# Kernel tuning notes

Measured on AMD Instinct MI355X. Metric: run time of the kernel, lower is better.

The kernel has to match this reference:

```python
import jax, jax.numpy as jnp
import numpy as np

B, F, ND, H, H1, M, NSEL = 8192, 40, 10, 64, 16, 75, 60
GRU_L = 3


def setup_inputs() -> dict:
    key = jax.random.key(0)
    ks = iter(jax.random.split(key, 64))
    def nrm(shape, scale=1.0):
        return jax.random.normal(next(ks), shape, jnp.float32) * scale
    d = {}
    d["X"] = nrm((B, 22, F))
    d["A"] = jax.random.uniform(next(ks), (B, 22, 22), dtype=jnp.float32)
    FO = F + (F - ND)  # 70: tiled R features + node-specific features
    for br, fin in (("R", F), ("O", FO), ("D", FO)):
        d[f"Wg_{br}"] = nrm((fin, H), fin ** -0.5)
        d[f"bg_{br}"] = jnp.zeros((H,), jnp.float32)
    for br, gin in (("R", 2 * H), ("O", 3 * H), ("D", 2 * H)):
        d[f"Wz_{br}"] = nrm((gin, H), gin ** -0.5)
        d[f"Wr_{br}"] = nrm((gin, H), gin ** -0.5)
        d[f"Wm_{br}"] = nrm((gin, H), gin ** -0.5)
        d[f"bm_{br}"] = jnp.zeros((H,), jnp.float32)
    for br in "ROD":
        d[f"W1_{br}"] = nrm((H, H1), H ** -0.5)
        d[f"b1_{br}"] = jnp.zeros((H1,), jnp.float32)
        d[f"W2_{br}"] = nrm((H1, 1), H1 ** -0.5)
    # temporal branch: 3 role-specific learned season vectors + fwd/bwd 1-unit GRUs
    d["temporal"] = nrm((3, M), 0.1)
    d["gru_k"] = nrm((3, 2, 3))      # [branch, fwd/bwd, (z,r,h)] input kernels (input dim 1)
    d["gru_rk"] = nrm((3, 2, 3))     # recurrent kernels (units=1)
    d["gru_b"] = jnp.zeros((3, 2, 2, 3), jnp.float32)  # reset_after=True: input & recurrent bias
    d["wout"] = nrm((3,))            # output Dense(1, no bias) on 1-dim GRU output
    d["ys_succ_ind"] = jnp.sort(jax.random.randint(next(ks), (NSEL,), 0, M))
    return d


def _temporal_probs(t, k, rk, b, wo, idx):
    # t:[M]  k,rk:[2,3]  b:[2,2,3]  wo: scalar. Keras GRU (units=1, reset_after=True).
    def make_step(kk, rkk, bb):
        def step(h, x):
            z = jax.nn.sigmoid(x * kk[0] + bb[0, 0] + h * rkk[0] + bb[1, 0])
            r = jax.nn.sigmoid(x * kk[1] + bb[0, 1] + h * rkk[1] + bb[1, 1])
            hh = jnp.tanh(x * kk[2] + bb[0, 2] + r * (h * rkk[2] + bb[1, 2]))
            hn = z * h + (1.0 - z) * hh
            return hn, hn
        return step
    h0 = jnp.zeros((), t.dtype)
    _, f = jax.lax.scan(make_step(k[0], rk[0], b[0]), h0, t)          # forward GRU
    _, g = jax.lax.scan(make_step(k[1], rk[1], b[1]), h0, f[::-1])     # go_backwards GRU (keeps reversed order, as Keras)
    p = jax.nn.softmax(g * wo)   # softmax over M time steps
    return p[idx]                # gather successful-season indices -> [NSEL]


def _fwd(X, A, Wg_R, bg_R, Wg_O, bg_O, Wg_D, bg_D,
         Wz_R, Wr_R, Wm_R, bm_R, Wz_O, Wr_O, Wm_O, bm_O,
         Wz_D, Wr_D, Wm_D, bm_D,
         W1_R, b1_R, W2_R, W1_O, b1_O, W2_O, W1_D, b1_D, W2_D,
         temporal, gru_k, gru_rk, gru_b, wout, ys_succ_ind):
    X_R = X[:, :1, :]                                               # [B,1,F]
    X_O = jnp.concatenate([jnp.tile(X_R, (1, 10, 1)), X[:, 1:11, ND:]], -1)  # [B,10,FO]
    X_D = jnp.concatenate([jnp.tile(X_R, (1, 11, 1)), X[:, 11:, ND:]], -1)   # [B,11,FO]
    A_RO = A[:, :1, 1:11]    # R <- O  [B,1,10]
    A_OR = A[:, 1:11, :1]    # O <- R  [B,10,1]
    A_OD = A[:, 1:11, 11:]   # O <- D  [B,10,11]
    A_DO = A[:, 11:, 1:11]   # D <- O  [B,11,10]
    h_R = jnp.tanh(X_R @ Wg_R + bg_R)
    h_O = jnp.tanh(X_O @ Wg_O + bg_O)
    h_D = jnp.tanh(X_D @ Wg_D + bg_D)
    def gate(h, n, Wz, Wr, Wm, bm):
        hn = jnp.concatenate([h, n], -1)
        z = jax.nn.sigmoid(hn @ Wz)
        r = jax.nn.sigmoid(hn @ Wr)
        hm = jnp.tanh(jnp.concatenate([h * r, n], -1) @ Wm + bm)
        return (1.0 - z) * h + z * hm
    for _ in range(GRU_L):
        n_R = A_RO @ h_O                                            # [B,1,H]
        n_O = jnp.concatenate([A_OR @ h_R, A_OD @ h_D], -1)         # [B,10,2H]
        n_D = A_DO @ h_O                                            # [B,11,H]
        h_R = gate(h_R, n_R, Wz_R, Wr_R, Wm_R, bm_R)
        h_O = gate(h_O, n_O, Wz_O, Wr_O, Wm_O, bm_O)
        h_D = gate(h_D, n_D, Wz_D, Wr_D, Wm_D, bm_D)
    s_R = (jnp.tanh(h_R @ W1_R + b1_R) @ W2_R)[:, 0]                # squeeze node dim -> [B,1]
    s_O = jnp.sum(jnp.tanh(h_O @ W1_O + b1_O) @ W2_O, axis=1)       # [B,1]
    s_D = jnp.sum(jnp.tanh(h_D @ W1_D + b1_D) @ W2_D, axis=1)       # [B,1]
    tp = jax.vmap(_temporal_probs, in_axes=(0, 0, 0, 0, 0, None))(
        temporal, gru_k, gru_rk, gru_b, wout, ys_succ_ind)          # [3,NSEL]
    return s_R * tp[0] + s_O * tp[1] + s_D * tp[2]                  # [B,NSEL]


def reference(X, A, Wg_R, bg_R, Wg_O, bg_O, Wg_D, bg_D,
              Wz_R, Wr_R, Wm_R, bm_R, Wz_O, Wr_O, Wm_O, bm_O,
              Wz_D, Wr_D, Wm_D, bm_D,
              W1_R, b1_R, W2_R, W1_O, b1_O, W2_O, W1_D, b1_D, W2_D,
              temporal, gru_k, gru_rk, gru_b, wout, ys_succ_ind):
    return _fwd(X, A, Wg_R, bg_R, Wg_O, bg_O, Wg_D, bg_D,
                Wz_R, Wr_R, Wm_R, bm_R, Wz_O, Wr_O, Wm_O, bm_O,
                Wz_D, Wr_D, Wm_D, bm_D,
                W1_R, b1_R, W2_R, W1_O, b1_O, W2_O, W1_D, b1_D, W2_D,
                temporal, gru_k, gru_rk, gru_b, wout, ys_succ_ind)
```

## Files before the change

### kernel.cpp

```cpp
#include <hip/hip_runtime.h>
#include <hip/hip_bf16.h>
#include <math.h>

#define DEV __device__ __forceinline__

DEV float sigmoidf_(float x) { return 1.0f / (1.0f + __expf(-x)); }

#define L5A(OP) OP(0,0) OP(1,1) OP(2,2) OP(3,3) OP(4,4)
#define L5B(OP) OP(0,5) OP(1,6) OP(2,7) OP(3,8) OP(4,9)
#define L6A(OP) OP(0,0) OP(1,1) OP(2,2) OP(3,3) OP(4,4) OP(5,5)
#define L5D(OP) OP(0,6) OP(1,7) OP(2,8) OP(3,9) OP(4,10)

#define AROB 0
#define AORB 16
#define AODB 32
#define ADOB 144
#define ANUM 256

DEV float gstep(float x, float h, const float* k, const float* rk, const float* bb) {
  const float z  = sigmoidf_(fmaf(x, k[0], bb[0]) + fmaf(h, rk[0], bb[3]));
  const float r  = sigmoidf_(fmaf(x, k[1], bb[1]) + fmaf(h, rk[1], bb[4]));
  const float hh = tanhf(fmaf(x, k[2], bb[2]) + r * fmaf(h, rk[2], bb[5]));
  return z * h + (1.f - z) * hh;
}

__global__ void __launch_bounds__(64, 1)
// ... 41 lines not shown
  else if (fi < 144) { W = WzO; base = 96;  }
  else if (fi < 192) { W = WrO; base = 144; }
  else if (fi < 240) { W = WmO; base = 192; }
  else if (fi < 272) { W = WzD; base = 240; }
  else if (fi < 304) { W = WrD; base = 272; }
  else               { W = WmD; base = 304; }
  const int kb = fi - base;
  float4 v;
  v.x = W[(kb * 4 + 0) * 64 + c];
  v.y = W[(kb * 4 + 1) * 64 + c];
  v.z = W[(kb * 4 + 2) * 64 + c];
  v.w = W[(kb * 4 + 3) * 64 + c];
  *(float4*)(ws + 1024 + (size_t)fi * 1024 + c * 16) = v;
}

#define ZRDECL(s,i) float az##s = 0.f, ar##s = 0.f;
#define AORD(s,i)  const float aor##s = sA2[AORB + (i)];
#define OS0(s,i) { const float4 v = *reinterpret_cast<const float4*>(&hS[(1+(i))*64 + kb*4]); \
  az##s=fmaf(v.x,wz.x,az##s); az##s=fmaf(v.y,wz.y,az##s); az##s=fmaf(v.z,wz.z,az##s); az##s=fmaf(v.w,wz.w,az##s); \
  ar##s=fmaf(v.x,wr.x,ar##s); ar##s=fmaf(v.y,wr.y,ar##s); ar##s=fmaf(v.z,wr.z,ar##s); ar##s=fmaf(v.w,wr.w,ar##s); }
#define OS1(s,i) { az##s=fmaf(aor##s,uz.x,az##s); az##s=fmaf(aor##s,uz.y,az##s); \
  az##s=fmaf(aor##s,uz.z,az##s); az##s=fmaf(aor##s,uz.w,az##s); \
  ar##s=fmaf(aor##s,ur.x,ar##s); ar##s=fmaf(aor##s,ur.y,ar##s); \
  ar##s=fmaf(aor##s,ur.z,ar##s); ar##s=fmaf(aor##s,ur.w,ar##s); }
#define OS2(s,i) { const float4 v = *reinterpret_cast<const float4*>(&nS[(1+(i))*64 + (kb-32)*4]); \
  az##s=fmaf(v.x,wz.x,az##s); az##s=fmaf(v.y,wz.y,az##s); az##s=fmaf(v.z,wz.z,az##s); az##s=fmaf(v.w,wz.w,az##s); \
  ar##s=fmaf(v.x,wr.x,ar##s); ar##s=fmaf(v.y,wr.y,ar##s); ar##s=fmaf(v.z,wr.z,ar##s); ar##s=fmaf(v.w,wr.w,ar##s); }
#define OSIG(s,i) zS##s = sigmoidf_(az##s); const float rr##s = sigmoidf_(ar##s);
#define OGST(s,i) gS[(1+(i))*64+c] = hS[(1+(i))*64+c] * rr##s;
#define OAMD(s,i) aS##s = bmOc;
#define OM0(s,i) { const float4 v = *reinterpret_cast<const float4*>(&gS[(1+(i))*64 + kb*4]); \
  aS##s=fmaf(v.x,wm.x,aS##s); aS##s=fmaf(v.y,wm.y,aS##s); aS##s=fmaf(v.z,wm.z,aS##s); aS##s=fmaf(v.w,wm.w,aS##s); }
#define OM1(s,i) { aS##s=fmaf(aor##s,um.x,aS##s); aS##s=fmaf(aor##s,um.y,aS##s); \
  aS##s=fmaf(aor##s,um.z,aS##s); aS##s=fmaf(aor##s,um.w,aS##s); }
#define OM2(s,i) { const float4 v = *reinterpret_cast<const float4*>(&nS[(1+(i))*64 + (kb-32)*4]); \
  aS##s=fmaf(v.x,wm.x,aS##s); aS##s=fmaf(v.y,wm.y,aS##s); aS##s=fmaf(v.z,wm.z,aS##s); aS##s=fmaf(v.w,wm.w,aS##s); }

#define DS0(s,i) { const float4 v = *reinterpret_cast<const float4*>(&hS[(11+(i))*64 + kb*4]); \
  az##s=fmaf(v.x,wz.x,az##s); az##s=fmaf(v.y,wz.y,az##s); az##s=fmaf(v.z,wz.z,az##s); az##s=fmaf(v.w,wz.w,az##s); \
  ar##s=fmaf(v.x,wr.x,ar##s); ar##s=fmaf(v.y,wr.y,ar##s); ar##s=fmaf(v.z,wr.z,ar##s); ar##s=fmaf(v.w,wr.w,ar##s); }
#define DS1(s,i) { const float4 v = *reinterpret_cast<const float4*>(&nS[(11+(i))*64 + (kb-16)*4]); \
  az##s=fmaf(v.x,wz.x,az##s); az##s=fmaf(v.y,wz.y,az##s); az##s=fmaf(v.z,wz.z,az##s); az##s=fmaf(v.w,wz.w,az##s); \
  ar##s=fmaf(v.x,wr.x,ar##s); ar##s=fmaf(v.y,wr.y,ar##s); ar##s=fmaf(v.z,wr.z,ar##s); ar##s=fmaf(v.w,wr.w,ar##s); }
#define DSIG(s,i) zS##s = sigmoidf_(az##s); const float rr##s = sigmoidf_(ar##s);
#define DGST(s,i) gS[(11+(i))*64+c] = hS[(11+(i))*64+c] * rr##s;
#define DAMD(s,i) aS##s = bmDc;
#define DM0(s,i) { const float4 v = *reinterpret_cast<const float4*>(&gS[(11+(i))*64 + kb*4]); \
  aS##s=fmaf(v.x,wm.x,aS##s); aS##s=fmaf(v.y,wm.y,aS##s); aS##s=fmaf(v.z,wm.z,aS##s); aS##s=fmaf(v.w,wm.w,aS##s); }
#define DM1(s,i) { const float4 v = *reinterpret_cast<const float4*>(&nS[(11+(i))*64 + (kb-16)*4]); \
  aS##s=fmaf(v.x,wm.x,aS##s); aS##s=fmaf(v.y,wm.y,aS##s); aS##s=fmaf(v.z,wm.z,aS##s); aS##s=fmaf(v.w,wm.w,aS##s); }

#define OGATE(LIST) { \
  LIST(ZRDECL) LIST(AORD) \
  _Pragma("unroll 2") for (int kb = 0; kb < 16; ++kb) { \
    const float4 wz = pWzO[kb*64+c], wr = pWrO[kb*64+c]; LIST(OS0) } \
  _Pragma("unroll 2") for (int kb = 16; kb < 32; ++kb) { \
    const float4 wz = pWzO[kb*64+c], wr = pWrO[kb*64+c]; \
    const float4 h0 = *reinterpret_cast<const float4*>(&hS[(kb-16)*4]); \
    float4 uz, ur; \
    uz.x=h0.x*wz.x; uz.y=h0.y*wz.y; uz.z=h0.z*wz.z; uz.w=h0.w*wz.w; \
    ur.x=h0.x*wr.x; ur.y=h0.y*wr.y; ur.z=h0.z*wr.z; ur.w=h0.w*wr.w; \
    LIST(OS1) } \
  _Pragma("unroll 2") for (int kb = 32; kb < 48; ++kb) { \
    const float4 wz = pWzO[kb*64+c], wr = pWrO[kb*64+c]; LIST(OS2) } \
  LIST(OSIG) LIST(OGST) LIST(OAMD) \
  _Pragma("unroll 2") for (int kb = 0; kb < 16; ++kb) { \
    const float4 wm = pWmO[kb*64+c]; LIST(OM0) } \
  _Pragma("unroll 2") for (int kb = 16; kb < 32; ++kb) { \
    const float4 wm = pWmO[kb*64+c]; \
    const float4 h0 = *reinterpret_cast<const float4*>(&hS[(kb-16)*4]); \
    float4 um; um.x=h0.x*wm.x; um.y=h0.y*wm.y; um.z=h0.z*wm.z; um.w=h0.w*wm.w; \
    LIST(OM1) } \
  _Pragma("unroll 2") for (int kb = 32; kb < 48; ++kb) { \
    const float4 wm = pWmO[kb*64+c]; LIST(OM2) } }

#define DGATE(LIST) { \
  LIST(ZRDECL) \
  _Pragma("unroll 2") for (int kb = 0; kb < 16; ++kb) { \
    const float4 wz = pWzD[kb*64+c], wr = pWrD[kb*64+c]; LIST(DS0) } \
  _Pragma("unroll 2") for (int kb = 16; kb < 32; ++kb) { \
    const float4 wz = pWzD[kb*64+c], wr = pWrD[kb*64+c]; LIST(DS1) } \
  LIST(DSIG) LIST(DGST) LIST(DAMD) \
  _Pragma("unroll 2") for (int kb = 0; kb < 16; ++kb) { \
    const float4 wm = pWmD[kb*64+c]; LIST(DM0) } \
  _Pragma("unroll 2") for (int kb = 16; kb < 32; ++kb) { \
    const float4 wm = pWmD[kb*64+c]; LIST(DM1) } }

#define OUPD(s,i) { const float h_ = hS[(1+(i))*64+c]; \
  hS[(1+(i))*64+c] = (1.f - zS##s)*h_ + zS##s*tanhf(aS##s); }
#define DUPD(s,i) { const float h_ = hS[(11+(i))*64+c]; \
  hS[(11+(i))*64+c] = (1.f - zS##s)*h_ + zS##s*tanhf(aS##s); }

#define NSO(s,i) nS[(1+(i))*64+c] = \
  sA2[AODB+(i)*11+0]*hd0 + sA2[AODB+(i)*11+1]*hd1 + sA2[AODB+(i)*11+2]*hd2 + sA2[AODB+(i)*11+3]*hd3 \
+ sA2[AODB+(i)*11+4]*hd4 + sA2[AODB+(i)*11+5]*hd5 + sA2[AODB+(i)*11+6]*hd6 + sA2[AODB+(i)*11+7]*hd7 \
+ sA2[AODB+(i)*11+8]*hd8 + sA2[AODB+(i)*11+9]*hd9 + sA2[AODB+(i)*11+10]*hd10;
#define NSD(s,i) nS[(11+(i))*64+c] = \
  sA2[ADOB+(i)*10+0]*ho0 + sA2[ADOB+(i)*10+1]*ho1 + sA2[ADOB+(i)*10+2]*ho2 + sA2[ADOB+(i)*10+3]*ho3 \
+ sA2[ADOB+(i)*10+4]*ho4 + sA2[ADOB+(i)*10+5]*ho5 + sA2[ADOB+(i)*10+6]*ho6 + sA2[ADOB+(i)*10+7]*ho7 \
+ sA2[ADOB+(i)*10+8]*ho8 + sA2[ADOB+(i)*10+9]*ho9;

__global__ void __launch_bounds__(256) ggnn_main(
    const float* __restrict__ X, const float* __restrict__ A,
    const float* __restrict__ WgR, const float* __restrict__ bgR,
    const float* __restrict__ WgO, const float* __restrict__ bgO,
    const float* __restrict__ WgD, const float* __restrict__ bgD,
    const float* __restrict__ bmR, const float* __restrict__ bmO, const float* __restrict__ bmD,
    const float* __restrict__ W1R, const float* __restrict__ b1R, const float* __restrict__ W2R,
    const float* __restrict__ W1O, const float* __restrict__ b1O, const float* __restrict__ W2O,
    const float* __restrict__ W1D, const float* __restrict__ b1D, const float* __restrict__ W2D,
    const char* __restrict__ ws, const float* __restrict__ tp,
    float* __restrict__ out) {
  const int b = blockIdx.x;
  const int w = threadIdx.x >> 6;
  const int c = threadIdx.x & 63;
  const int tid = threadIdx.x;

  __shared__ __align__(16) float hS[22 * 64];
  __shared__ __align__(16) float nS[22 * 64];
  __shared__ __align__(16) float gS[22 * 64];
  __shared__ float sA2[ANUM];
  __shared__ float red[16];

  const float4* pk = (const float4*)(ws + 1024);
  const float4* pWzR = pk + 0   * 64;
  const float4* pWrR = pk + 32  * 64;
  const float4* pWmR = pk + 64  * 64;
  const float4* pWzO = pk + 96  * 64;
  const float4* pWrO = pk + 144 * 64;
  const float4* pWmO = pk + 192 * 64;
  const float4* pWzD = pk + 240 * 64;
  const float4* pWrD = pk + 272 * 64;
  const float4* pWmD = pk + 304 * 64;

  const float* Xb = X + (size_t)b * 880;
  const float* Ab = A + (size_t)b * 484;
  for (int t = tid; t < 880; t += 256) gS[t] = Xb[t];
  if (tid < 10) {
    sA2[AROB + tid] = Ab[1 + tid];
    sA2[AORB + tid] = Ab[(1 + tid) * 22];
  }
  for (int t = tid; t < 110; t += 256) {
    const int i = t / 11, j = t - i * 11;
    sA2[AODB + t] = Ab[(1 + i) * 22 + 11 + j];
  }
  for (int t = tid; t < 110; t += 256) {
    const int i = t / 10, j = t - i * 10;
    sA2[ADOB + t] = Ab[(11 + i) * 22 + 1 + j];
  }
  __syncthreads();

  if (w == 0 || w == 1) {
    float cO = bgO[c];
#pragma unroll 4
    for (int k = 0; k < 40; ++k) cO = fmaf(gS[k], WgO[k * 64 + c], cO);
    float a0 = cO, a1 = cO, a2 = cO, a3 = cO, a4 = cO;
    const int r0 = (w == 0) ? 1 : 6;
#pragma unroll 2
    for (int k = 0; k < 30; ++k) {
      const float wo_ = WgO[(40 + k) * 64 + c];
      a0 = fmaf(gS[(r0 + 0) * 40 + 10 + k], wo_, a0);
      a1 = fmaf(gS[(r0 + 1) * 40 + 10 + k], wo_, a1);
      a2 = fmaf(gS[(r0 + 2) * 40 + 10 + k], wo_, a2);
      a3 = fmaf(gS[(r0 + 3) * 40 + 10 + k], wo_, a3);
      a4 = fmaf(gS[(r0 + 4) * 40 + 10 + k], wo_, a4);
    }
    hS[(r0 + 0) * 64 + c] = tanhf(a0);
    hS[(r0 + 1) * 64 + c] = tanhf(a1);
    hS[(r0 + 2) * 64 + c] = tanhf(a2);
    hS[(r0 + 3) * 64 + c] = tanhf(a3);
    hS[(r0 + 4) * 64 + c] = tanhf(a4);
  } else {
    float cD = bgD[c];
#pragma unroll 4
    for (int k = 0; k < 40; ++k) cD = fmaf(gS[k], WgD[k * 64 + c], cD);
    if (w == 2) {
      float a0 = cD, a1 = cD, a2 = cD, a3 = cD, a4 = cD, a5 = cD;
#pragma unroll 2
      for (int k = 0; k < 30; ++k) {
        const float wd_ = WgD[(40 + k) * 64 + c];
        a0 = fmaf(gS[11 * 40 + 10 + k], wd_, a0);
        a1 = fmaf(gS[12 * 40 + 10 + k], wd_, a1);
        a2 = fmaf(gS[13 * 40 + 10 + k], wd_, a2);
        a3 = fmaf(gS[14 * 40 + 10 + k], wd_, a3);
        a4 = fmaf(gS[15 * 40 + 10 + k], wd_, a4);
        a5 = fmaf(gS[16 * 40 + 10 + k], wd_, a5);
      }
      hS[11 * 64 + c] = tanhf(a0); hS[12 * 64 + c] = tanhf(a1);
      hS[13 * 64 + c] = tanhf(a2); hS[14 * 64 + c] = tanhf(a3);
      hS[15 * 64 + c] = tanhf(a4); hS[16 * 64 + c] = tanhf(a5);
    } else {
      float a0 = cD, a1 = cD, a2 = cD, a3 = cD, a4 = cD;
#pragma unroll 2
      for (int k = 0; k < 30; ++k) {
        const float wd_ = WgD[(40 + k) * 64 + c];
        a0 = fmaf(gS[17 * 40 + 10 + k], wd_, a0);
        a1 = fmaf(gS[18 * 40 + 10 + k], wd_, a1);
        a2 = fmaf(gS[19 * 40 + 10 + k], wd_, a2);
        a3 = fmaf(gS[20 * 40 + 10 + k], wd_, a3);
        a4 = fmaf(gS[21 * 40 + 10 + k], wd_, a4);
      }
      hS[17 * 64 + c] = tanhf(a0); hS[18 * 64 + c] = tanhf(a1);
      hS[19 * 64 + c] = tanhf(a2); hS[20 * 64 + c] = tanhf(a3);
      hS[21 * 64 + c] = tanhf(a4);
      float aR = bgR[c];
#pragma unroll 4
      for (int k = 0; k < 40; ++k) aR = fmaf(gS[k], WgR[k * 64 + c], aR);
      hS[c] = tanhf(aR);
    }
  }
  __syncthreads();

  const float bmOc = bmO[c], bmDc = bmD[c], bmRc = bmR[c];
  float zS0 = 0.f, zS1 = 0.f, zS2 = 0.f, zS3 = 0.f, zS4 = 0.f, zS5 = 0.f;
  float aS0 = 0.f, aS1 = 0.f, aS2 = 0.f, aS3 = 0.f, aS4 = 0.f, aS5 = 0.f;

  for (int it = 0; it < 3; ++it) {
    if (w == 0 || w == 1) {
      const float hd0 = hS[11*64+c], hd1 = hS[12*64+c], hd2 = hS[13*64+c], hd3 = hS[14*64+c];
      const float hd4 = hS[15*64+c], hd5 = hS[16*64+c], hd6 = hS[17*64+c], hd7 = hS[18*64+c];
      const float hd8 = hS[19*64+c], hd9 = hS[20*64+c], hd10 = hS[21*64+c];
      if (w == 0) { L5A(NSO) } else { L5B(NSO) }
    } else {
      const float ho0 = hS[1*64+c], ho1 = hS[2*64+c], ho2 = hS[3*64+c], ho3 = hS[4*64+c];
      const float ho4 = hS[5*64+c], ho5 = hS[6*64+c], ho6 = hS[7*64+c], ho7 = hS[8*64+c];
      const float ho8 = hS[9*64+c], ho9 = hS[10*64+c];
      if (w == 2) { L6A(NSD) }
      else {
        L5D(NSD)
        nS[c] = sA2[AROB+0]*ho0 + sA2[AROB+1]*ho1 + sA2[AROB+2]*ho2 + sA2[AROB+3]*ho3
              + sA2[AROB+4]*ho4 + sA2[AROB+5]*ho5 + sA2[AROB+6]*ho6 + sA2[AROB+7]*ho7
              + sA2[AROB+8]*ho8 + sA2[AROB+9]*ho9;
      }
    }

    if (w == 0)      { OGATE(L5A) }
    else if (w == 1) { OGATE(L5B) }
    else if (w == 2) { DGATE(L6A) }
    else {
      DGATE(L5D)
      {
        float azr = 0.f, arr = 0.f;
#pragma unroll 2
        for (int kb = 0; kb < 16; ++kb) {
          const float4 wz = pWzR[kb*64+c], wr = pWrR[kb*64+c];
          const float4 v = *reinterpret_cast<const float4*>(&hS[kb*4]);
          azr=fmaf(v.x,wz.x,azr); azr=fmaf(v.y,wz.y,azr); azr=fmaf(v.z,wz.z,azr); azr=fmaf(v.w,wz.w,azr);
          arr=fmaf(v.x,wr.x,arr); arr=fmaf(v.y,wr.y,arr); arr=fmaf(v.z,wr.z,arr); arr=fmaf(v.w,wr.w,arr);
        }
#pragma unroll 2
        for (int kb = 16; kb < 32; ++kb) {
          const float4 wz = pWzR[kb*64+c], wr = pWrR[kb*64+c];
          const float4 v = *reinterpret_cast<const float4*>(&nS[(kb-16)*4]);
          azr=fmaf(v.x,wz.x,azr); azr=fmaf(v.y,wz.y,azr); azr=fmaf(v.z,wz.z,azr); azr=fmaf(v.w,wz.w,azr);
          arr=fmaf(v.x,wr.x,arr); arr=fmaf(v.y,wr.y,arr); arr=fmaf(v.z,wr.z,arr); arr=fmaf(v.w,wr.w,arr);
        }
        zS5 = sigmoidf_(azr);
        const float r5 = sigmoidf_(arr);
        gS[c] = hS[c] * r5;
        aS5 = bmRc;
#pragma unroll 2
        for (int kb = 0; kb < 16; ++kb) {
          const float4 wm = pWmR[kb*64+c];
          const float4 v = *reinterpret_cast<const float4*>(&gS[kb*4]);
          aS5=fmaf(v.x,wm.x,aS5); aS5=fmaf(v.y,wm.y,aS5); aS5=fmaf(v.z,wm.z,aS5); aS5=fmaf(v.w,wm.w,aS5);
        }
#pragma unroll 2
        for (int kb = 16; kb < 32; ++kb) {
          const float4 wm = pWmR[kb*64+c];
          const float4 v = *reinterpret_cast<const float4*>(&nS[(kb-16)*4]);
          aS5=fmaf(v.x,wm.x,aS5); aS5=fmaf(v.y,wm.y,aS5); aS5=fmaf(v.z,wm.z,aS5); aS5=fmaf(v.w,wm.w,aS5);
        }
      }
    }

    __syncthreads();

    if (w == 0)      { L5A(OUPD) }
    else if (w == 1) { L5B(OUPD) }
    else if (w == 2) { L6A(DUPD) }
    else {
      L5D(DUPD)
      { const float h_ = hS[c]; hS[c] = (1.f - zS5) * h_ + zS5 * tanhf(aS5); }
    }
    __syncthreads();
  }

  const int g = c >> 4;
  const int c1 = c & 15;
  float pR = 0.f, pO = 0.f, pD = 0.f;
  int lo, hi;
  if      (w == 0) { lo = 1;  hi = 6;  }
  else if (w == 1) { lo = 6;  hi = 11; }
  else if (w == 2) { lo = 11; hi = 17; }
  else             { lo = 17; hi = 22; }
  for (int rr = lo + g; rr < hi; rr += 4) {
    const float* W1; const float* b1; const float* W2;
    if (rr < 11) { W1 = W1O; b1 = b1O; W2 = W2O; }
// ... 88 lines not shown
```

Measured before the change: 829.1 us.

## Keep GGNN node states in registers and broadcast via readlane instead of LDS

Each wave now holds its node hidden states, neighbor messages and reset-gated states in registers and broadcasts the k-th element across lanes with readlane inside the gate matvecs. This replaces the float4 shared-memory reads of hS, nS and gS, and it drops the nS and gS buffers. The only shared state left is hS, used for cross-wave exchange. The change also moves the barrier to after the message computation, so the update writes to hS no longer need a separate sync. In exchange, readlane issues many scalar reads that each have to wait on VALU results, and more state now lives in registers.

```diff
diff --git a/kernel.cpp b/kernel.cpp
--- a/kernel.cpp
+++ b/kernel.cpp
@@ -6,10 +6,12 @@
 
 DEV float sigmoidf_(float x) { return 1.0f / (1.0f + __expf(-x)); }
 
-#define L5A(OP) OP(0,0) OP(1,1) OP(2,2) OP(3,3) OP(4,4)
-#define L5B(OP) OP(0,5) OP(1,6) OP(2,7) OP(3,8) OP(4,9)
-#define L6A(OP) OP(0,0) OP(1,1) OP(2,2) OP(3,3) OP(4,4) OP(5,5)
-#define L5D(OP) OP(0,6) OP(1,7) OP(2,8) OP(3,9) OP(4,10)
+DEV float RLf(float v, int lane) {
+  return __int_as_float(__builtin_amdgcn_readlane(__float_as_int(v), lane));
+}
+
+#define LO(OP) OP(0) OP(1) OP(2) OP(3) OP(4)
+#define L6(OP) OP(0) OP(1) OP(2) OP(3) OP(4) OP(5)
 
 #define AROB 0
 #define AORB 16
@@ -81,92 +83,6 @@
   *(float4*)(ws + 1024 + (size_t)fi * 1024 + c * 16) = v;
 }
 
-#define ZRDECL(s,i) float az##s = 0.f, ar##s = 0.f;
-#define AORD(s,i)  const float aor##s = sA2[AORB + (i)];
-#define OS0(s,i) { const float4 v = *reinterpret_cast<const float4*>(&hS[(1+(i))*64 + kb*4]); \
-  az##s=fmaf(v.x,wz.x,az##s); az##s=fmaf(v.y,wz.y,az##s); az##s=fmaf(v.z,wz.z,az##s); az##s=fmaf(v.w,wz.w,az##s); \
-  ar##s=fmaf(v.x,wr.x,ar##s); ar##s=fmaf(v.y,wr.y,ar##s); ar##s=fmaf(v.z,wr.z,ar##s); ar##s=fmaf(v.w,wr.w,ar##s); }
-#define OS1(s,i) { az##s=fmaf(aor##s,uz.x,az##s); az##s=fmaf(aor##s,uz.y,az##s); \
-  az##s=fmaf(aor##s,uz.z,az##s); az##s=fmaf(aor##s,uz.w,az##s); \
-  ar##s=fmaf(aor##s,ur.x,ar##s); ar##s=fmaf(aor##s,ur.y,ar##s); \
-  ar##s=fmaf(aor##s,ur.z,ar##s); ar##s=fmaf(aor##s,ur.w,ar##s); }
-#define OS2(s,i) { const float4 v = *reinterpret_cast<const float4*>(&nS[(1+(i))*64 + (kb-32)*4]); \
-  az##s=fmaf(v.x,wz.x,az##s); az##s=fmaf(v.y,wz.y,az##s); az##s=fmaf(v.z,wz.z,az##s); az##s=fmaf(v.w,wz.w,az##s); \
-  ar##s=fmaf(v.x,wr.x,ar##s); ar##s=fmaf(v.y,wr.y,ar##s); ar##s=fmaf(v.z,wr.z,ar##s); ar##s=fmaf(v.w,wr.w,ar##s); }
-#define OSIG(s,i) zS##s = sigmoidf_(az##s); const float rr##s = sigmoidf_(ar##s);
-#define OGST(s,i) gS[(1+(i))*64+c] = hS[(1+(i))*64+c] * rr##s;
-#define OAMD(s,i) aS##s = bmOc;
-#define OM0(s,i) { const float4 v = *reinterpret_cast<const float4*>(&gS[(1+(i))*64 + kb*4]); \
-  aS##s=fmaf(v.x,wm.x,aS##s); aS##s=fmaf(v.y,wm.y,aS##s); aS##s=fmaf(v.z,wm.z,aS##s); aS##s=fmaf(v.w,wm.w,aS##s); }
-#define OM1(s,i) { aS##s=fmaf(aor##s,um.x,aS##s); aS##s=fmaf(aor##s,um.y,aS##s); \
-  aS##s=fmaf(aor##s,um.z,aS##s); aS##s=fmaf(aor##s,um.w,aS##s); }
-#define OM2(s,i) { const float4 v = *reinterpret_cast<const float4*>(&nS[(1+(i))*64 + (kb-32)*4]); \
-  aS##s=fmaf(v.x,wm.x,aS##s); aS##s=fmaf(v.y,wm.y,aS##s); aS##s=fmaf(v.z,wm.z,aS##s); aS##s=fmaf(v.w,wm.w,aS##s); }
-
-#define DS0(s,i) { const float4 v = *reinterpret_cast<const float4*>(&hS[(11+(i))*64 + kb*4]); \
-  az##s=fmaf(v.x,wz.x,az##s); az##s=fmaf(v.y,wz.y,az##s); az##s=fmaf(v.z,wz.z,az##s); az##s=fmaf(v.w,wz.w,az##s); \
-  ar##s=fmaf(v.x,wr.x,ar##s); ar##s=fmaf(v.y,wr.y,ar##s); ar##s=fmaf(v.z,wr.z,ar##s); ar##s=fmaf(v.w,wr.w,ar##s); }
-#define DS1(s,i) { const float4 v = *reinterpret_cast<const float4*>(&nS[(11+(i))*64 + (kb-16)*4]); \
-  az##s=fmaf(v.x,wz.x,az##s); az##s=fmaf(v.y,wz.y,az##s); az##s=fmaf(v.z,wz.z,az##s); az##s=fmaf(v.w,wz.w,az##s); \
-  ar##s=fmaf(v.x,wr.x,ar##s); ar##s=fmaf(v.y,wr.y,ar##s); ar##s=fmaf(v.z,wr.z,ar##s); ar##s=fmaf(v.w,wr.w,ar##s); }
-#define DSIG(s,i) zS##s = sigmoidf_(az##s); const float rr##s = sigmoidf_(ar##s);
-#define DGST(s,i) gS[(11+(i))*64+c] = hS[(11+(i))*64+c] * rr##s;
-#define DAMD(s,i) aS##s = bmDc;
-#define DM0(s,i) { const float4 v = *reinterpret_cast<const float4*>(&gS[(11+(i))*64 + kb*4]); \
-  aS##s=fmaf(v.x,wm.x,aS##s); aS##s=fmaf(v.y,wm.y,aS##s); aS##s=fmaf(v.z,wm.z,aS##s); aS##s=fmaf(v.w,wm.w,aS##s); }
-#define DM1(s,i) { const float4 v = *reinterpret_cast<const float4*>(&nS[(11+(i))*64 + (kb-16)*4]); \
-  aS##s=fmaf(v.x,wm.x,aS##s); aS##s=fmaf(v.y,wm.y,aS##s); aS##s=fmaf(v.z,wm.z,aS##s); aS##s=fmaf(v.w,wm.w,aS##s); }
-
-#define OGATE(LIST) { \
-  LIST(ZRDECL) LIST(AORD) \
-  _Pragma("unroll 2") for (int kb = 0; kb < 16; ++kb) { \
-    const float4 wz = pWzO[kb*64+c], wr = pWrO[kb*64+c]; LIST(OS0) } \
-  _Pragma("unroll 2") for (int kb = 16; kb < 32; ++kb) { \
-    const float4 wz = pWzO[kb*64+c], wr = pWrO[kb*64+c]; \
-    const float4 h0 = *reinterpret_cast<const float4*>(&hS[(kb-16)*4]); \
-    float4 uz, ur; \
-    uz.x=h0.x*wz.x; uz.y=h0.y*wz.y; uz.z=h0.z*wz.z; uz.w=h0.w*wz.w; \
-    ur.x=h0.x*wr.x; ur.y=h0.y*wr.y; ur.z=h0.z*wr.z; ur.w=h0.w*wr.w; \
-    LIST(OS1) } \
-  _Pragma("unroll 2") for (int kb = 32; kb < 48; ++kb) { \
-    const float4 wz = pWzO[kb*64+c], wr = pWrO[kb*64+c]; LIST(OS2) } \
-  LIST(OSIG) LIST(OGST) LIST(OAMD) \
-  _Pragma("unroll 2") for (int kb = 0; kb < 16; ++kb) { \
-    const float4 wm = pWmO[kb*64+c]; LIST(OM0) } \
-  _Pragma("unroll 2") for (int kb = 16; kb < 32; ++kb) { \
-    const float4 wm = pWmO[kb*64+c]; \
-    const float4 h0 = *reinterpret_cast<const float4*>(&hS[(kb-16)*4]); \
-    float4 um; um.x=h0.x*wm.x; um.y=h0.y*wm.y; um.z=h0.z*wm.z; um.w=h0.w*wm.w; \
-    LIST(OM1) } \
-  _Pragma("unroll 2") for (int kb = 32; kb < 48; ++kb) { \
-    const float4 wm = pWmO[kb*64+c]; LIST(OM2) } }
-
-#define DGATE(LIST) { \
-  LIST(ZRDECL) \
-  _Pragma("unroll 2") for (int kb = 0; kb < 16; ++kb) { \
-    const float4 wz = pWzD[kb*64+c], wr = pWrD[kb*64+c]; LIST(DS0) } \
-  _Pragma("unroll 2") for (int kb = 16; kb < 32; ++kb) { \
-    const float4 wz = pWzD[kb*64+c], wr = pWrD[kb*64+c]; LIST(DS1) } \
-  LIST(DSIG) LIST(DGST) LIST(DAMD) \
-  _Pragma("unroll 2") for (int kb = 0; kb < 16; ++kb) { \
-    const float4 wm = pWmD[kb*64+c]; LIST(DM0) } \
-  _Pragma("unroll 2") for (int kb = 16; kb < 32; ++kb) { \
-    const float4 wm = pWmD[kb*64+c]; LIST(DM1) } }
-
-#define OUPD(s,i) { const float h_ = hS[(1+(i))*64+c]; \
-  hS[(1+(i))*64+c] = (1.f - zS##s)*h_ + zS##s*tanhf(aS##s); }
-#define DUPD(s,i) { const float h_ = hS[(11+(i))*64+c]; \
-  hS[(11+(i))*64+c] = (1.f - zS##s)*h_ + zS##s*tanhf(aS##s); }
-
-#define NSO(s,i) nS[(1+(i))*64+c] = \
-  sA2[AODB+(i)*11+0]*hd0 + sA2[AODB+(i)*11+1]*hd1 + sA2[AODB+(i)*11+2]*hd2 + sA2[AODB+(i)*11+3]*hd3 \
-+ sA2[AODB+(i)*11+4]*hd4 + sA2[AODB+(i)*11+5]*hd5 + sA2[AODB+(i)*11+6]*hd6 + sA2[AODB+(i)*11+7]*hd7 \
-+ sA2[AODB+(i)*11+8]*hd8 + sA2[AODB+(i)*11+9]*hd9 + sA2[AODB+(i)*11+10]*hd10;
-#define NSD(s,i) nS[(11+(i))*64+c] = \
-  sA2[ADOB+(i)*10+0]*ho0 + sA2[ADOB+(i)*10+1]*ho1 + sA2[ADOB+(i)*10+2]*ho2 + sA2[ADOB+(i)*10+3]*ho3 \
-+ sA2[ADOB+(i)*10+4]*ho4 + sA2[ADOB+(i)*10+5]*ho5 + sA2[ADOB+(i)*10+6]*ho6 + sA2[ADOB+(i)*10+7]*ho7 \
-+ sA2[ADOB+(i)*10+8]*ho8 + sA2[ADOB+(i)*10+9]*ho9;
-
 __global__ void __launch_bounds__(256) ggnn_main(
     const float* __restrict__ X, const float* __restrict__ A,
     const float* __restrict__ WgR, const float* __restrict__ bgR,
@@ -183,9 +99,8 @@
   const int c = threadIdx.x & 63;
   const int tid = threadIdx.x;
 
+  __shared__ __align__(16) float xS[896];
   __shared__ __align__(16) float hS[22 * 64];
-  __shared__ __align__(16) float nS[22 * 64];
-  __shared__ __align__(16) float gS[22 * 64];
   __shared__ float sA2[ANUM];
   __shared__ float red[16];
 
@@ -202,7 +117,7 @@
 
   const float* Xb = X + (size_t)b * 880;
   const float* Ab = A + (size_t)b * 484;
-  for (int t = tid; t < 880; t += 256) gS[t] = Xb[t];
+  for (int t = tid; t < 880; t += 256) xS[t] = Xb[t];
   if (tid < 10) {
     sA2[AROB + tid] = Ab[1 + tid];
     sA2[AORB + tid] = Ab[(1 + tid) * 22];
@@ -217,138 +132,310 @@
   }
   __syncthreads();
 
-  if (w == 0 || w == 1) {
+  float h0, h1, h2, h3, h4, h5;
+  float hRreg = 0.f;
+
+  if (w < 2) {
     float cO = bgO[c];
 #pragma unroll 4
-    for (int k = 0; k < 40; ++k) cO = fmaf(gS[k], WgO[k * 64 + c], cO);
+    for (int k = 0; k < 40; ++k) cO = fmaf(xS[k], WgO[k * 64 + c], cO);
     float a0 = cO, a1 = cO, a2 = cO, a3 = cO, a4 = cO;
-    const int r0 = (w == 0) ? 1 : 6;
+    const int r0 = 1 + w * 5;
 #pragma unroll 2
     for (int k = 0; k < 30; ++k) {
       const float wo_ = WgO[(40 + k) * 64 + c];
-      a0 = fmaf(gS[(r0 + 0) * 40 + 10 + k], wo_, a0);
-      a1 = fmaf(gS[(r0 + 1) * 40 + 10 + k], wo_, a1);
-      a2 = fmaf(gS[(r0 + 2) * 40 + 10 + k], wo_, a2);
-      a3 = fmaf(gS[(r0 + 3) * 40 + 10 + k], wo_, a3);
-      a4 = fmaf(gS[(r0 + 4) * 40 + 10 + k], wo_, a4);
-    }
-    hS[(r0 + 0) * 64 + c] = tanhf(a0);
-    hS[(r0 + 1) * 64 + c] = tanhf(a1);
-    hS[(r0 + 2) * 64 + c] = tanhf(a2);
-    hS[(r0 + 3) * 64 + c] = tanhf(a3);
-    hS[(r0 + 4) * 64 + c] = tanhf(a4);
+      a0 = fmaf(xS[(r0 + 0) * 40 + 10 + k], wo_, a0);
+      a1 = fmaf(xS[(r0 + 1) * 40 + 10 + k], wo_, a1);
+      a2 = fmaf(xS[(r0 + 2) * 40 + 10 + k], wo_, a2);
+      a3 = fmaf(xS[(r0 + 3) * 40 + 10 + k], wo_, a3);
+      a4 = fmaf(xS[(r0 + 4) * 40 + 10 + k], wo_, a4);
+    }
+    h0 = tanhf(a0); h1 = tanhf(a1); h2 = tanhf(a2); h3 = tanhf(a3); h4 = tanhf(a4);
+    hS[(r0 + 0) * 64 + c] = h0; hS[(r0 + 1) * 64 + c] = h1;
+    hS[(r0 + 2) * 64 + c] = h2; hS[(r0 + 3) * 64 + c] = h3;
+    hS[(r0 + 4) * 64 + c] = h4;
   } else {
     float cD = bgD[c];
 #pragma unroll 4
-    for (int k = 0; k < 40; ++k) cD = fmaf(gS[k], WgD[k * 64 + c], cD);
+    for (int k = 0; k < 40; ++k) cD = fmaf(xS[k], WgD[k * 64 + c], cD);
     if (w == 2) {
       float a0 = cD, a1 = cD, a2 = cD, a3 = cD, a4 = cD, a5 = cD;
 #pragma unroll 2
       for (int k = 0; k < 30; ++k) {
         const float wd_ = WgD[(40 + k) * 64 + c];
-        a0 = fmaf(gS[11 * 40 + 10 + k], wd_, a0);
-        a1 = fmaf(gS[12 * 40 + 10 + k], wd_, a1);
-        a2 = fmaf(gS[13 * 40 + 10 + k], wd_, a2);
-        a3 = fmaf(gS[14 * 40 + 10 + k], wd_, a3);
-        a4 = fmaf(gS[15 * 40 + 10 + k], wd_, a4);
-        a5 = fmaf(gS[16 * 40 + 10 + k], wd_, a5);
-      }
-      hS[11 * 64 + c] = tanhf(a0); hS[12 * 64 + c] = tanhf(a1);
-      hS[13 * 64 + c] = tanhf(a2); hS[14 * 64 + c] = tanhf(a3);
-      hS[15 * 64 + c] = tanhf(a4); hS[16 * 64 + c] = tanhf(a5);
+        a0 = fmaf(xS[11 * 40 + 10 + k], wd_, a0);
+        a1 = fmaf(xS[12 * 40 + 10 + k], wd_, a1);
+        a2 = fmaf(xS[13 * 40 + 10 + k], wd_, a2);
+        a3 = fmaf(xS[14 * 40 + 10 + k], wd_, a3);
+        a4 = fmaf(xS[15 * 40 + 10 + k], wd_, a4);
+        a5 = fmaf(xS[16 * 40 + 10 + k], wd_, a5);
+      }
+      h0 = tanhf(a0); h1 = tanhf(a1); h2 = tanhf(a2);
+      h3 = tanhf(a3); h4 = tanhf(a4); h5 = tanhf(a5);
+      hS[11 * 64 + c] = h0; hS[12 * 64 + c] = h1; hS[13 * 64 + c] = h2;
+      hS[14 * 64 + c] = h3; hS[15 * 64 + c] = h4; hS[16 * 64 + c] = h5;
     } else {
       float a0 = cD, a1 = cD, a2 = cD, a3 = cD, a4 = cD;
 #pragma unroll 2
       for (int k = 0; k < 30; ++k) {
         const float wd_ = WgD[(40 + k) * 64 + c];
-        a0 = fmaf(gS[17 * 40 + 10 + k], wd_, a0);
-        a1 = fmaf(gS[18 * 40 + 10 + k], wd_, a1);
-        a2 = fmaf(gS[19 * 40 + 10 + k], wd_, a2);
-        a3 = fmaf(gS[20 * 40 + 10 + k], wd_, a3);
-        a4 = fmaf(gS[21 * 40 + 10 + k], wd_, a4);
-      }
-      hS[17 * 64 + c] = tanhf(a0); hS[18 * 64 + c] = tanhf(a1);
-      hS[19 * 64 + c] = tanhf(a2); hS[20 * 64 + c] = tanhf(a3);
-      hS[21 * 64 + c] = tanhf(a4);
+        a0 = fmaf(xS[17 * 40 + 10 + k], wd_, a0);
+        a1 = fmaf(xS[18 * 40 + 10 + k], wd_, a1);
+        a2 = fmaf(xS[19 * 40 + 10 + k], wd_, a2);
+        a3 = fmaf(xS[20 * 40 + 10 + k], wd_, a3);
+        a4 = fmaf(xS[21 * 40 + 10 + k], wd_, a4);
+      }
+      h0 = tanhf(a0); h1 = tanhf(a1); h2 = tanhf(a2); h3 = tanhf(a3); h4 = tanhf(a4);
+      hS[17 * 64 + c] = h0; hS[18 * 64 + c] = h1; hS[19 * 64 + c] = h2;
+      hS[20 * 64 + c] = h3; hS[21 * 64 + c] = h4;
       float aR = bgR[c];
 #pragma unroll 4
-      for (int k = 0; k < 40; ++k) aR = fmaf(gS[k], WgR[k * 64 + c], aR);
-      hS[c] = tanhf(aR);
+      for (int k = 0; k < 40; ++k) aR = fmaf(xS[k], WgR[k * 64 + c], aR);
+      hRreg = tanhf(aR);
+      hS[c] = hRreg;
     }
   }
   __syncthreads();
 
   const float bmOc = bmO[c], bmDc = bmD[c], bmRc = bmR[c];
-  float zS0 = 0.f, zS1 = 0.f, zS2 = 0.f, zS3 = 0.f, zS4 = 0.f, zS5 = 0.f;
-  float aS0 = 0.f, aS1 = 0.f, aS2 = 0.f, aS3 = 0.f, aS4 = 0.f, aS5 = 0.f;
 
   for (int it = 0; it < 3; ++it) {
-    if (w == 0 || w == 1) {
-      const float hd0 = hS[11*64+c], hd1 = hS[12*64+c], hd2 = hS[13*64+c], hd3 = hS[14*64+c];
-      const float hd4 = hS[15*64+c], hd5 = hS[16*64+c], hd6 = hS[17*64+c], hd7 = hS[18*64+c];
-      const float hd8 = hS[19*64+c], hd9 = hS[20*64+c], hd10 = hS[21*64+c];
-      if (w == 0) { L5A(NSO) } else { L5B(NSO) }
+    const float hRl = hS[c];
+    float nn0 = 0.f, nn1 = 0.f, nn2 = 0.f, nn3 = 0.f, nn4 = 0.f, nn5 = 0.f;
+    float nRv = 0.f;
+
+    if (w < 2) {
+      const float hd0 = hS[11*64+c], hd1 = hS[12*64+c], hd2 = hS[13*64+c];
+      const float hd3 = hS[14*64+c], hd4 = hS[15*64+c], hd5 = hS[16*64+c];
+      const float hd6 = hS[17*64+c], hd7 = hS[18*64+c], hd8 = hS[19*64+c];
+      const float hd9 = hS[20*64+c], hd10 = hS[21*64+c];
+      const int a0 = w * 5;
+#define NN(s) nn##s = sA2[AODB+(a0+s)*11+0]*hd0 + sA2[AODB+(a0+s)*11+1]*hd1 \
+  + sA2[AODB+(a0+s)*11+2]*hd2 + sA2[AODB+(a0+s)*11+3]*hd3 + sA2[AODB+(a0+s)*11+4]*hd4 \
+  + sA2[AODB+(a0+s)*11+5]*hd5 + sA2[AODB+(a0+s)*11+6]*hd6 + sA2[AODB+(a0+s)*11+7]*hd7 \
+  + sA2[AODB+(a0+s)*11+8]*hd8 + sA2[AODB+(a0+s)*11+9]*hd9 + sA2[AODB+(a0+s)*11+10]*hd10;
+      LO(NN)
+#undef NN
     } else {
-      const float ho0 = hS[1*64+c], ho1 = hS[2*64+c], ho2 = hS[3*64+c], ho3 = hS[4*64+c];
-      const float ho4 = hS[5*64+c], ho5 = hS[6*64+c], ho6 = hS[7*64+c], ho7 = hS[8*64+c];
-      const float ho8 = hS[9*64+c], ho9 = hS[10*64+c];
-      if (w == 2) { L6A(NSD) }
-      else {
-        L5D(NSD)
-        nS[c] = sA2[AROB+0]*ho0 + sA2[AROB+1]*ho1 + sA2[AROB+2]*ho2 + sA2[AROB+3]*ho3
-              + sA2[AROB+4]*ho4 + sA2[AROB+5]*ho5 + sA2[AROB+6]*ho6 + sA2[AROB+7]*ho7
-              + sA2[AROB+8]*ho8 + sA2[AROB+9]*ho9;
-      }
-    }
-
-    if (w == 0)      { OGATE(L5A) }
-    else if (w == 1) { OGATE(L5B) }
-    else if (w == 2) { DGATE(L6A) }
-    else {
-      DGATE(L5D)
-      {
-        float azr = 0.f, arr = 0.f;
-#pragma unroll 2
-        for (int kb = 0; kb < 16; ++kb) {
-          const float4 wz = pWzR[kb*64+c], wr = pWrR[kb*64+c];
-          const float4 v = *reinterpret_cast<const float4*>(&hS[kb*4]);
-          azr=fmaf(v.x,wz.x,azr); azr=fmaf(v.y,wz.y,azr); azr=fmaf(v.z,wz.z,azr); azr=fmaf(v.w,wz.w,azr);
-          arr=fmaf(v.x,wr.x,arr); arr=fmaf(v.y,wr.y,arr); arr=fmaf(v.z,wr.z,arr); arr=fmaf(v.w,wr.w,arr);
-        }
-#pragma unroll 2
-        for (int kb = 16; kb < 32; ++kb) {
-          const float4 wz = pWzR[kb*64+c], wr = pWrR[kb*64+c];
-          const float4 v = *reinterpret_cast<const float4*>(&nS[(kb-16)*4]);
-          azr=fmaf(v.x,wz.x,azr); azr=fmaf(v.y,wz.y,azr); azr=fmaf(v.z,wz.z,azr); azr=fmaf(v.w,wz.w,azr);
-          arr=fmaf(v.x,wr.x,arr); arr=fmaf(v.y,wr.y,arr); arr=fmaf(v.z,wr.z,arr); arr=fmaf(v.w,wr.w,arr);
-        }
-        zS5 = sigmoidf_(azr);
-        const float r5 = sigmoidf_(arr);
-        gS[c] = hS[c] * r5;
-        aS5 = bmRc;
-#pragma unroll 2
-        for (int kb = 0; kb < 16; ++kb) {
-          const float4 wm = pWmR[kb*64+c];
-          const float4 v = *reinterpret_cast<const float4*>(&gS[kb*4]);
-          aS5=fmaf(v.x,wm.x,aS5); aS5=fmaf(v.y,wm.y,aS5); aS5=fmaf(v.z,wm.z,aS5); aS5=fmaf(v.w,wm.w,aS5);
-        }
-#pragma unroll 2
-        for (int kb = 16; kb < 32; ++kb) {
-          const float4 wm = pWmR[kb*64+c];
-          const float4 v = *reinterpret_cast<const float4*>(&nS[(kb-16)*4]);
-          aS5=fmaf(v.x,wm.x,aS5); aS5=fmaf(v.y,wm.y,aS5); aS5=fmaf(v.z,wm.z,aS5); aS5=fmaf(v.w,wm.w,aS5);
-        }
-      }
-    }
-
+      const float ho0 = hS[1*64+c], ho1 = hS[2*64+c], ho2 = hS[3*64+c];
+      const float ho3 = hS[4*64+c], ho4 = hS[5*64+c], ho5 = hS[6*64+c];
+      const float ho6 = hS[7*64+c], ho7 = hS[8*64+c], ho8 = hS[9*64+c];
+      const float ho9 = hS[10*64+c];
+      const int adx = (w == 2) ? 0 : 6;
+      if (w == 2) {
+#define NN(s) nn##s = sA2[ADOB+(adx+s)*10+0]*ho0 + sA2[ADOB+(adx+s)*10+1]*ho1 \
+  + sA2[ADOB+(adx+s)*10+2]*ho2 + sA2[ADOB+(adx+s)*10+3]*ho3 + sA2[ADOB+(adx+s)*10+4]*ho4 \
+  + sA2[ADOB+(adx+s)*10+5]*ho5 + sA2[ADOB+(adx+s)*10+6]*ho6 + sA2[ADOB+(adx+s)*10+7]*ho7 \
+  + sA2[ADOB+(adx+s)*10+8]*ho8 + sA2[ADOB+(adx+s)*10+9]*ho9;
+        L6(NN)
+#undef NN
+      } else {
+#define NN(s) nn##s = sA2[ADOB+(adx+s)*10+0]*ho0 + sA2[ADOB+(adx+s)*10+1]*ho1 \
+  + sA2[ADOB+(adx+s)*10+2]*ho2 + sA2[ADOB+(adx+s)*10+3]*ho3 + sA2[ADOB+(adx+s)*10+4]*ho4 \
+  + sA2[ADOB+(adx+s)*10+5]*ho5 + sA2[ADOB+(adx+s)*10+6]*ho6 + sA2[ADOB+(adx+s)*10+7]*ho7 \
+  + sA2[ADOB+(adx+s)*10+8]*ho8 + sA2[ADOB+(adx+s)*10+9]*ho9;
+        LO(NN)
+#undef NN
+        nRv = sA2[AROB+0]*ho0 + sA2[AROB+1]*ho1 + sA2[AROB+2]*ho2 + sA2[AROB+3]*ho3
+            + sA2[AROB+4]*ho4 + sA2[AROB+5]*ho5 + sA2[AROB+6]*ho6 + sA2[AROB+7]*ho7
+            + sA2[AROB+8]*ho8 + sA2[AROB+9]*ho9;
+      }
+    }
     __syncthreads();
 
-    if (w == 0)      { L5A(OUPD) }
-    else if (w == 1) { L5B(OUPD) }
-    else if (w == 2) { L6A(DUPD) }
-    else {
-      L5D(DUPD)
-      { const float h_ = hS[c]; hS[c] = (1.f - zS5) * h_ + zS5 * tanhf(aS5); }
+    if (w < 2) {
+      const int a0 = w * 5;
+      const float aor0 = sA2[AORB+a0+0], aor1 = sA2[AORB+a0+1], aor2 = sA2[AORB+a0+2];
+      const float aor3 = sA2[AORB+a0+3], aor4 = sA2[AORB+a0+4];
+      float az0=0.f,az1=0.f,az2=0.f,az3=0.f,az4=0.f;
+      float ar0=0.f,ar1=0.f,ar2=0.f,ar3=0.f,ar4=0.f;
+#pragma unroll 2
+      for (int kb = 0; kb < 16; ++kb) {
+        const float4 wz = pWzO[kb*64+c], wr = pWrO[kb*64+c];
+        const int k4 = kb*4;
+#define OPX(s) { const float t0=RLf(h##s,k4), t1=RLf(h##s,k4+1), t2=RLf(h##s,k4+2), t3=RLf(h##s,k4+3); \
+  az##s=fmaf(t0,wz.x,az##s); az##s=fmaf(t1,wz.y,az##s); az##s=fmaf(t2,wz.z,az##s); az##s=fmaf(t3,wz.w,az##s); \
+  ar##s=fmaf(t0,wr.x,ar##s); ar##s=fmaf(t1,wr.y,ar##s); ar##s=fmaf(t2,wr.z,ar##s); ar##s=fmaf(t3,wr.w,ar##s); }
+        LO(OPX)
+#undef OPX
+      }
+#pragma unroll 2
+      for (int kb = 16; kb < 32; ++kb) {
+        const float4 wz = pWzO[kb*64+c], wr = pWrO[kb*64+c];
+        const int k4 = (kb-16)*4;
+        const float u0=RLf(hRl,k4), u1=RLf(hRl,k4+1), u2=RLf(hRl,k4+2), u3=RLf(hRl,k4+3);
+        const float uz0=u0*wz.x, uz1=u1*wz.y, uz2=u2*wz.z, uz3=u3*wz.w;
+        const float ur0=u0*wr.x, ur1=u1*wr.y, ur2=u2*wr.z, ur3=u3*wr.w;
+#define OPX(s) { az##s=fmaf(aor##s,uz0,az##s); az##s=fmaf(aor##s,uz1,az##s); \
+  az##s=fmaf(aor##s,uz2,az##s); az##s=fmaf(aor##s,uz3,az##s); \
+  ar##s=fmaf(aor##s,ur0,ar##s); ar##s=fmaf(aor##s,ur1,ar##s); \
+  ar##s=fmaf(aor##s,ur2,ar##s); ar##s=fmaf(aor##s,ur3,ar##s); }
+        LO(OPX)
+#undef OPX
+      }
+#pragma unroll 2
+      for (int kb = 32; kb < 48; ++kb) {
+        const float4 wz = pWzO[kb*64+c], wr = pWrO[kb*64+c];
+        const int k4 = (kb-32)*4;
+#define OPX(s) { const float t0=RLf(nn##s,k4), t1=RLf(nn##s,k4+1), t2=RLf(nn##s,k4+2), t3=RLf(nn##s,k4+3); \
+  az##s=fmaf(t0,wz.x,az##s); az##s=fmaf(t1,wz.y,az##s); az##s=fmaf(t2,wz.z,az##s); az##s=fmaf(t3,wz.w,az##s); \
+  ar##s=fmaf(t0,wr.x,ar##s); ar##s=fmaf(t1,wr.y,ar##s); ar##s=fmaf(t2,wr.z,ar##s); ar##s=fmaf(t3,wr.w,ar##s); }
+        LO(OPX)
+#undef OPX
+      }
+#define OPX(s) const float z##s = sigmoidf_(az##s); const float hro##s = h##s * sigmoidf_(ar##s);
+      LO(OPX)
+#undef OPX
+      float aS0=bmOc, aS1=bmOc, aS2=bmOc, aS3=bmOc, aS4=bmOc;
+#pragma unroll 2
+      for (int kb = 0; kb < 16; ++kb) {
+        const float4 wm = pWmO[kb*64+c];
+        const int k4 = kb*4;
+#define OPX(s) { const float t0=RLf(hro##s,k4), t1=RLf(hro##s,k4+1), t2=RLf(hro##s,k4+2), t3=RLf(hro##s,k4+3); \
+  aS##s=fmaf(t0,wm.x,aS##s); aS##s=fmaf(t1,wm.y,aS##s); aS##s=fmaf(t2,wm.z,aS##s); aS##s=fmaf(t3,wm.w,aS##s); }
+        LO(OPX)
+#undef OPX
+      }
+#pragma unroll 2
+      for (int kb = 16; kb < 32; ++kb) {
+        const float4 wm = pWmO[kb*64+c];
+        const int k4 = (kb-16)*4;
+        const float u0=RLf(hRl,k4), u1=RLf(hRl,k4+1), u2=RLf(hRl,k4+2), u3=RLf(hRl,k4+3);
+        const float um0=u0*wm.x, um1=u1*wm.y, um2=u2*wm.z, um3=u3*wm.w;
+#define OPX(s) { aS##s=fmaf(aor##s,um0,aS##s); aS##s=fmaf(aor##s,um1,aS##s); \
+  aS##s=fmaf(aor##s,um2,aS##s); aS##s=fmaf(aor##s,um3,aS##s); }
+        LO(OPX)
+#undef OPX
+      }
+#pragma unroll 2
+      for (int kb = 32; kb < 48; ++kb) {
+        const float4 wm = pWmO[kb*64+c];
+        const int k4 = (kb-32)*4;
+#define OPX(s) { const float t0=RLf(nn##s,k4), t1=RLf(nn##s,k4+1), t2=RLf(nn##s,k4+2), t3=RLf(nn##s,k4+3); \
+  aS##s=fmaf(t0,wm.x,aS##s); aS##s=fmaf(t1,wm.y,aS##s); aS##s=fmaf(t2,wm.z,aS##s); aS##s=fmaf(t3,wm.w,aS##s); }
+        LO(OPX)
+#undef OPX
+      }
+      const int r0 = 1 + a0;
+#define OPX(s) { h##s = (1.f - z##s)*h##s + z##s*tanhf(aS##s); hS[(r0+s)*64+c] = h##s; }
+      LO(OPX)
+#undef OPX
+    } else if (w == 2) {
+      float az0=0.f,az1=0.f,az2=0.f,az3=0.f,az4=0.f,az5=0.f;
+      float ar0=0.f,ar1=0.f,ar2=0.f,ar3=0.f,ar4=0.f,ar5=0.f;
+#pragma unroll 2
+      for (int kb = 0; kb < 16; ++kb) {
+        const float4 wz = pWzD[kb*64+c], wr = pWrD[kb*64+c];
+        const int k4 = kb*4;
+#define OPX(s) { const float t0=RLf(h##s,k4), t1=RLf(h##s,k4+1), t2=RLf(h##s,k4+2), t3=RLf(h##s,k4+3); \
+  az##s=fmaf(t0,wz.x,az##s); az##s=fmaf(t1,wz.y,az##s); az##s=fmaf(t2,wz.z,az##s); az##s=fmaf(t3,wz.w,az##s); \
+  ar##s=fmaf(t0,wr.x,ar##s); ar##s=fmaf(t1,wr.y,ar##s); ar##s=fmaf(t2,wr.z,ar##s); ar##s=fmaf(t3,wr.w,ar##s); }
+        L6(OPX)
+#undef OPX
+      }
+#pragma unroll 2
+      for (int kb = 16; kb < 32; ++kb) {
+        const float4 wz = pWzD[kb*64+c], wr = pWrD[kb*64+c];
+        const int k4 = (kb-16)*4;
+#define OPX(s) { const float t0=RLf(nn##s,k4), t1=RLf(nn##s,k4+1), t2=RLf(nn##s,k4+2), t3=RLf(nn##s,k4+3); \
+  az##s=fmaf(t0,wz.x,az##s); az##s=fmaf(t1,wz.y,az##s); az##s=fmaf(t2,wz.z,az##s); az##s=fmaf(t3,wz.w,az##s); \
+  ar##s=fmaf(t0,wr.x,ar##s); ar##s=fmaf(t1,wr.y,ar##s); ar##s=fmaf(t2,wr.z,ar##s); ar##s=fmaf(t3,wr.w,ar##s); }
+        L6(OPX)
+#undef OPX
+      }
+#define OPX(s) const float z##s = sigmoidf_(az##s); const float hrd##s = h##s * sigmoidf_(ar##s);
+      L6(OPX)
+#undef OPX
+      float aS0=bmDc, aS1=bmDc, aS2=bmDc, aS3=bmDc, aS4=bmDc, aS5=bmDc;
+#pragma unroll 2
+      for (int kb = 0; kb < 16; ++kb) {
+        const float4 wm = pWmD[kb*64+c];
+        const int k4 = kb*4;
+#define OPX(s) { const float t0=RLf(hrd##s,k4), t1=RLf(hrd##s,k4+1), t2=RLf(hrd##s,k4+2), t3=RLf(hrd##s,k4+3); \
+  aS##s=fmaf(t0,wm.x,aS##s); aS##s=fmaf(t1,wm.y,aS##s); aS##s=fmaf(t2,wm.z,aS##s); aS##s=fmaf(t3,wm.w,aS##s); }
+        L6(OPX)
+#undef OPX
+      }
+#pragma unroll 2
+      for (int kb = 16; kb < 32; ++kb) {
+        const float4 wm = pWmD[kb*64+c];
+        const int k4 = (kb-16)*4;
+#define OPX(s) { const float t0=RLf(nn##s,k4), t1=RLf(nn##s,k4+1), t2=RLf(nn##s,k4+2), t3=RLf(nn##s,k4+3); \
+  aS##s=fmaf(t0,wm.x,aS##s); aS##s=fmaf(t1,wm.y,aS##s); aS##s=fmaf(t2,wm.z,aS##s); aS##s=fmaf(t3,wm.w,aS##s); }
+        L6(OPX)
+#undef OPX
+      }
+#define OPX(s) { h##s = (1.f - z##s)*h##s + z##s*tanhf(aS##s); hS[(11+s)*64+c] = h##s; }
+      L6(OPX)
+#undef OPX
+    } else {
+      float az0=0.f,az1=0.f,az2=0.f,az3=0.f,az4=0.f;
+      float ar0=0.f,ar1=0.f,ar2=0.f,ar3=0.f,ar4=0.f;
+      float azr = 0.f, arr = 0.f;
+#pragma unroll 2
+      for (int kb = 0; kb < 16; ++kb) {
+        const float4 wz = pWzD[kb*64+c], wr = pWrD[kb*64+c];
+        const int k4 = kb*4;
+#define OPX(s) { const float t0=RLf(h##s,k4), t1=RLf(h##s,k4+1), t2=RLf(h##s,k4+2), t3=RLf(h##s,k4+3); \
+  az##s=fmaf(t0,wz.x,az##s); az##s=fmaf(t1,wz.y,az##s); az##s=fmaf(t2,wz.z,az##s); az##s=fmaf(t3,wz.w,az##s); \
+  ar##s=fmaf(t0,wr.x,ar##s); ar##s=fmaf(t1,wr.y,ar##s); ar##s=fmaf(t2,wr.z,ar##s); ar##s=fmaf(t3,wr.w,ar##s); }
+        LO(OPX)
+#undef OPX
+        const float4 wzr = pWzR[kb*64+c], wrr = pWrR[kb*64+c];
+        const float q0=RLf(hRreg,k4), q1=RLf(hRreg,k4+1), q2=RLf(hRreg,k4+2), q3=RLf(hRreg,k4+3);
+        azr=fmaf(q0,wzr.x,azr); azr=fmaf(q1,wzr.y,azr); azr=fmaf(q2,wzr.z,azr); azr=fmaf(q3,wzr.w,azr);
+        arr=fmaf(q0,wrr.x,arr); arr=fmaf(q1,wrr.y,arr); arr=fmaf(q2,wrr.z,arr); arr=fmaf(q3,wrr.w,arr);
+      }
+#pragma unroll 2
+      for (int kb = 16; kb < 32; ++kb) {
+        const float4 wz = pWzD[kb*64+c], wr = pWrD[kb*64+c];
+        const int k4 = (kb-16)*4;
+#define OPX(s) { const float t0=RLf(nn##s,k4), t1=RLf(nn##s,k4+1), t2=RLf(nn##s,k4+2), t3=RLf(nn##s,k4+3); \
+  az##s=fmaf(t0,wz.x,az##s); az##s=fmaf(t1,wz.y,az##s); az##s=fmaf(t2,wz.z,az##s); az##s=fmaf(t3,wz.w,az##s); \
+  ar##s=fmaf(t0,wr.x,ar##s); ar##s=fmaf(t1,wr.y,ar##s); ar##s=fmaf(t2,wr.z,ar##s); ar##s=fmaf(t3,wr.w,ar##s); }
+        LO(OPX)
+#undef OPX
+        const float4 wzr = pWzR[kb*64+c], wrr = pWrR[kb*64+c];
+        const float q0=RLf(nRv,k4), q1=RLf(nRv,k4+1), q2=RLf(nRv,k4+2), q3=RLf(nRv,k4+3);
+        azr=fmaf(q0,wzr.x,azr); azr=fmaf(q1,wzr.y,azr); azr=fmaf(q2,wzr.z,azr); azr=fmaf(q3,wzr.w,azr);
+        arr=fmaf(q0,wrr.x,arr); arr=fmaf(q1,wrr.y,arr); arr=fmaf(q2,wrr.z,arr); arr=fmaf(q3,wrr.w,arr);
+      }
+#define OPX(s) const float z##s = sigmoidf_(az##s); const float hrd##s = h##s * sigmoidf_(ar##s);
+      LO(OPX)
+#undef OPX
+      const float zr = sigmoidf_(azr);
+      const float hrr = hRreg * sigmoidf_(arr);
+      float aS0=bmDc, aS1=bmDc, aS2=bmDc, aS3=bmDc, aS4=bmDc;
+      float amr = bmRc;
+#pragma unroll 2
+      for (int kb = 0; kb < 16; ++kb) {
+        const float4 wm = pWmD[kb*64+c];
+        const int k4 = kb*4;
+#define OPX(s) { const float t0=RLf(hrd##s,k4), t1=RLf(hrd##s,k4+1), t2=RLf(hrd##s,k4+2), t3=RLf(hrd##s,k4+3); \
+  aS##s=fmaf(t0,wm.x,aS##s); aS##s=fmaf(t1,wm.y,aS##s); aS##s=fmaf(t2,wm.z,aS##s); aS##s=fmaf(t3,wm.w,aS##s); }
+        LO(OPX)
+#undef OPX
+        const float4 wmr = pWmR[kb*64+c];
+        const float q0=RLf(hrr,k4), q1=RLf(hrr,k4+1), q2=RLf(hrr,k4+2), q3=RLf(hrr,k4+3);
+        amr=fmaf(q0,wmr.x,amr); amr=fmaf(q1,wmr.y,amr); amr=fmaf(q2,wmr.z,amr); amr=fmaf(q3,wmr.w,amr);
+      }
+#pragma unroll 2
+      for (int kb = 16; kb < 32; ++kb) {
+        const float4 wm = pWmD[kb*64+c];
+        const int k4 = (kb-16)*4;
+#define OPX(s) { const float t0=RLf(nn##s,k4), t1=RLf(nn##s,k4+1), t2=RLf(nn##s,k4+2), t3=RLf(nn##s,k4+3); \
+  aS##s=fmaf(t0,wm.x,aS##s); aS##s=fmaf(t1,wm.y,aS##s); aS##s=fmaf(t2,wm.z,aS##s); aS##s=fmaf(t3,wm.w,aS##s); }
+        LO(OPX)
+#undef OPX
+        const float4 wmr = pWmR[kb*64+c];
+        const float q0=RLf(nRv,k4), q1=RLf(nRv,k4+1), q2=RLf(nRv,k4+2), q3=RLf(nRv,k4+3);
+        amr=fmaf(q0,wmr.x,amr); amr=fmaf(q1,wmr.y,amr); amr=fmaf(q2,wmr.z,amr); amr=fmaf(q3,wmr.w,amr);
+      }
+#define OPX(s) { h##s = (1.f - z##s)*h##s + z##s*tanhf(aS##s); hS[(17+s)*64+c] = h##s; }
+      LO(OPX)
+#undef OPX
+      hRreg = (1.f - zr) * hRreg + zr * tanhf(amr);
+      hS[c] = hRreg;
     }
     __syncthreads();
   }
```

New measurement: 1.045 ms. +26.0%, slower.
